# Kernel tuning notes

Measured on AMD Instinct MI355X. Metric: run time of the kernel, lower is better.

## Reference

```python
import jax, jax.numpy as jnp
import numpy as np

B, L, K, E, D, H = 16, 512, 48, 128, 384, 128

def _gelu(x):
    return jax.nn.gelu(x, approximate=False)  # torch nn.GELU default is erf-based

def setup_inputs() -> dict:
    key = jax.random.key(0)
    ks = jax.random.split(key, 16)
    def randn(k, shape, scale=1.0):
        return jax.random.normal(k, shape, dtype=jnp.float32) * scale
    inp = {
        "h_V": randn(ks[0], (B, L, D)),
        "h_E": randn(ks[1], (B, L, K, E)),
        "mask": jnp.ones((B, L), dtype=jnp.float32),
        "fw1": randn(ks[2], (E, D), 1.0 / np.sqrt(E)),
        "fb1": randn(ks[3], (D,), 0.02),
        "fw2": randn(ks[4], (D, D), 1.0 / np.sqrt(D)),
        "fb2": randn(ks[5], (D,), 0.02),
        "hw1": randn(ks[6], (D, H), 1.0 / np.sqrt(D)),
        "hb1": randn(ks[7], (H,), 0.02),
        "hw2": randn(ks[8], (H, H // 2), 1.0 / np.sqrt(H)),
        "hb2": randn(ks[9], (H // 2,), 0.02),
        "hw3": randn(ks[10], (H // 2, 1), 1.0 / np.sqrt(H // 2)),
        "hb3": randn(ks[11], (1,), 0.02),
        "E_idx": jax.random.randint(ks[12], (B, L, K), 0, L),
    }
    return inp

def reference(h_V, h_E, mask, fw1, fb1, fw2, fb2, hw1, hb1, hw2, hb2, hw3, hb3, E_idx):
    # CFConv: edge-conditioned filters [B,L,K,D]
    W = _gelu(_gelu(h_E @ fw1 + fb1) @ fw2 + fb2)
    # gather_nodes: x_j[b,l,k,:] = h_V[b, E_idx[b,l,k], :]
    x_j = jax.vmap(lambda x, idx: x[idx])(h_V, E_idx)  # [B,L,K,D]
    h = jnp.sum(x_j * W, axis=2)  # weighted sum over neighbors -> [B,L,D]
    # mlp_head (dropout = identity at inference)
    h = _gelu(h @ hw1 + hb1)
    h = _gelu(h @ hw2 + hb2)
    dG = (h @ hw3 + hb3)[..., 0]  # [B,L]
    valid_length = jnp.clip(jnp.sum(mask, axis=1), 1.0, None)  # [B]
    return jnp.sum(dG * mask, axis=1) / jnp.sqrt(valid_length)  # [B]
```

## Files before the change

kernel.cpp:

```cpp
#include <hip/hip_runtime.h>
#include <hip/hip_bf16.h>
#include <math.h>

#define NB 16
#define NL 512
#define NK 48
#define NE 128
#define ND 384
#define NH 128

typedef __attribute__((ext_vector_type(8))) short short8;
typedef __attribute__((ext_vector_type(4))) float f32x4;

__device__ __forceinline__ float gelu_fast(float x) {
    float t = x * fmaf(x * x, -0.1029437f, -2.3022087f);
    float e = __builtin_amdgcn_exp2f(t);
    return x * __builtin_amdgcn_rcpf(1.0f + e);
}

__device__ __forceinline__ unsigned short f2bf(float x) {
    union { float f; unsigned u; } v; v.f = x;
    unsigned r = v.u + 0x7fffu + ((v.u >> 16) & 1u);
    return (unsigned short)(r >> 16);
}

__device__ __forceinline__ unsigned short f2bf_rhu(float x) {
    union { float f; unsigned u; } v; v.f = x;
    return (unsigned short)((v.u + 0x8000u) >> 16);
}

__device__ __forceinline__ unsigned pk_bf16(float a, float b) {
    union { float f; unsigned u; } ua, ub; ua.f = a; ub.f = b;
    return __builtin_amdgcn_perm(ua.u + 0x8000u, ub.u + 0x8000u, 0x07060302u);
}

__global__ void pack_weights(const float* __restrict__ fw1,
                             const float* __restrict__ fw2,
                             const float* __restrict__ hw1,
                             const float* __restrict__ hw2,
                             unsigned short* __restrict__ fw1p,
                             unsigned short* __restrict__ fw2p,
                             unsigned short* __restrict__ hw1p,
                             unsigned short* __restrict__ hw2p,
                             float* __restrict__ dGsum) {
    int tid = blockIdx.x * 256 + threadIdx.x;
    if (tid < NB) dGsum[tid] = 0.0f;
    if (tid < NE * ND) {
        int k = tid / ND, n = tid % ND;
        int dst = (((k >> 5) * 24 + (n >> 4)) * 64 + ((k >> 3) & 3) * 16 + (n & 15)) * 8 + (k & 7);
        fw1p[dst] = f2bf(fw1[tid]);
    } else if (tid < NE * ND + ND * ND) {
        int i = tid - NE * ND;
        int k = i / ND, n = i % ND;
        int dst = (((k >> 5) * 24 + (n >> 4)) * 64 + ((k >> 3) & 3) * 16 + (n & 15)) * 8 + (k & 7);
        fw2p[dst] = f2bf(fw2[i]);
    } else if (tid < NE * ND + ND * ND + ND * NH) {
        int i = tid - (NE * ND + ND * ND);
        int k = i / NH, n = i % NH;
        int dst = (((k >> 5) * 8 + (n >> 4)) * 64 + ((k >> 3) & 3) * 16 + (n & 15)) * 8 + (k & 7);
        hw1p[dst] = f2bf(hw1[i]);
    } else if (tid < NE * ND + ND * ND + ND * NH + NH * (NH / 2)) {
        int i = tid - (NE * ND + ND * ND + ND * NH);
        int k = i / (NH / 2), n = i % (NH / 2);
        int dst = (((k >> 5) * 4 + (n >> 4)) * 64 + ((k >> 3) & 3) * 16 + (n & 15)) * 8 + (k & 7);
        hw2p[dst] = f2bf(hw2[i]);
    }
}

__global__ __launch_bounds__(256, 2) void cfconv_kernel(
    const float* __restrict__ h_V, const float* __restrict__ h_E,
    const float* __restrict__ fb1, const float* __restrict__ fb2,
    const unsigned short* __restrict__ fw1p,
    const unsigned short* __restrict__ fw2p,
    const int* __restrict__ E_idx, unsigned short* __restrict__ hbufB)
{
    __shared__ unsigned short smem[96 * 392];
    __shared__ int rowoff_s[96];

    const int t = threadIdx.x;
    const int wave = t >> 6, lane = t & 63;
    const int quad = lane >> 4, l16 = lane & 15;
    const int bl0 = blockIdx.x * 2;
    const int wn0 = wave * 96;

    if (t < 96) {
        int g = t / 48, k = t - g * 48;
        int bl = bl0 + g;
        int idx = E_idx[bl * NK + k];
        rowoff_s[t] = ((bl >> 9) * NL + idx) * ND;
    }

    {
        const float4* src = (const float4*)(h_E + (size_t)bl0 * (NK * NE));
        #pragma unroll
        for (int i = 0; i < 12; i++) {
            int v = i * 256 + t;
            float4 d = src[v];
            int r = v >> 5;
            int c = (v & 31) * 4;
            uint2 u;
            u.x = pk_bf16(d.y, d.x);
            u.y = pk_bf16(d.w, d.z);
            *(uint2*)&smem[r * 136 + c] = u;
        }
    }
    __syncthreads();

    f32x4 acc[6][6];

    #pragma unroll
    for (int mt = 0; mt < 6; mt++)
        #pragma unroll
        for (int nt = 0; nt < 6; nt++)
            acc[mt][nt] = (f32x4){0.f, 0.f, 0.f, 0.f};

    #pragma unroll
    for (int kt = 0; kt < 4; kt++) {
        short8 bfrag[6], afrag[6];
        #pragma unroll
        for (int nt = 0; nt < 6; nt++)
            bfrag[nt] = *(const short8*)(fw1p + (size_t)((kt * 24 + (wn0 >> 4) + nt) * 64 + lane) * 8);
        #pragma unroll
        for (int mt = 0; mt < 6; mt++)
            afrag[mt] = *(const short8*)&smem[(mt * 16 + l16) * 136 + kt * 32 + quad * 8];
        #pragma unroll
        for (int mt = 0; mt < 6; mt++)
            #pragma unroll
            for (int nt = 0; nt < 6; nt++)
                acc[mt][nt] = __builtin_amdgcn_mfma_f32_16x16x32_bf16(
                    afrag[mt], bfrag[nt], acc[mt][nt], 0, 0, 0);
    }
    __syncthreads();

    #pragma unroll
    for (int nt = 0; nt < 6; nt++) {
        int col = wn0 + nt * 16 + l16;
        float b1 = fb1[col];
        #pragma unroll
        for (int mt = 0; mt < 6; mt++) {
            int rowb = mt * 16 + quad * 4;
            #pragma unroll
            for (int r = 0; r < 4; r++)
                smem[(rowb + r) * 392 + col] = f2bf_rhu(gelu_fast(acc[mt][nt][r] + b1));
        }
    }
    __syncthreads();

    #pragma unroll
    for (int mt = 0; mt < 6; mt++)
        #pragma unroll
        for (int nt = 0; nt < 6; nt++)
            acc[mt][nt] = (f32x4){0.f, 0.f, 0.f, 0.f};

    for (int kt = 0; kt < 12; kt++) {
        short8 bfrag[6], afrag[6];
        #pragma unroll
        for (int nt = 0; nt < 6; nt++)
            bfrag[nt] = *(const short8*)(fw2p + (size_t)((kt * 24 + (wn0 >> 4) + nt) * 64 + lane) * 8);
        #pragma unroll
        for (int mt = 0; mt < 6; mt++)
            afrag[mt] = *(const short8*)&smem[(mt * 16 + l16) * 392 + kt * 32 + quad * 8];
        #pragma unroll
        for (int mt = 0; mt < 6; mt++)
            #pragma unroll
            for (int nt = 0; nt < 6; nt++)
                acc[mt][nt] = __builtin_amdgcn_mfma_f32_16x16x32_bf16(
                    afrag[mt], bfrag[nt], acc[mt][nt], 0, 0, 0);
    }

    float b2v[6];
    #pragma unroll
    for (int nt = 0; nt < 6; nt++) b2v[nt] = fb2[wn0 + nt * 16 + l16];

    #pragma unroll
    for (int g = 0; g < 2; g++) {
        const float* pv[12];
        #pragma unroll
        for (int mm = 0; mm < 3; mm++)
            #pragma unroll
            for (int r = 0; r < 4; r++)
                pv[mm * 4 + r] = h_V + rowoff_s[(g * 3 + mm) * 16 + quad * 4 + r] + wn0 + l16;

        #pragma unroll
        for (int nt = 0; nt < 6; nt++) {
            float s = 0.f;
            #pragma unroll
            for (int mm = 0; mm < 3; mm++) {
                #pragma unroll
                for (int r = 0; r < 4; r++) {
                    float w = gelu_fast(acc[g * 3 + mm][nt][r] + b2v[nt]);
                    s = fmaf(w, pv[mm * 4 + r][nt * 16], s);
                }
            }
            s += __shfl_xor(s, 16, 64);
            s += __shfl_xor(s, 32, 64);
            if (lane < 16)
                hbufB[(size_t)(bl0 + g) * ND + wn0 + nt * 16 + lane] = f2bf(s);
        }
    }
}

__global__ __launch_bounds__(64) void head_kernel(
    const unsigned short* __restrict__ hbufB,
    const unsigned short* __restrict__ hw1p, const float* __restrict__ hb1,
    const unsigned short* __restrict__ hw2p, const float* __restrict__ hb2,
    const float* __restrict__ hw3, const float* __restrict__ hb3,
    const float* __restrict__ mask, float* __restrict__ dGsum)
{
    __shared__ unsigned short T1[16 * 136];
    const int lane = threadIdx.x;
    const int quad = lane >> 4, l16 = lane & 15;
    const int row0 = blockIdx.x * 16;

    f32x4 acc1[8];
    #pragma unroll
    for (int nt = 0; nt < 8; nt++) acc1[nt] = (f32x4){0.f, 0.f, 0.f, 0.f};

    for (int kt = 0; kt < 12; kt++) {
        short8 a = *(const short8*)(hbufB + (size_t)(row0 + l16) * ND + kt * 32 + quad * 8);
        #pragma unroll
        for (int nt = 0; nt < 8; nt++) {
            short8 b = *(const short8*)(hw1p + (size_t)((kt * 8 + nt) * 64 + lane) * 8);
            acc1[nt] = __builtin_amdgcn_mfma_f32_16x16x32_bf16(a, b, acc1[nt], 0, 0, 0);
        }
    }

    #pragma unroll
    for (int nt = 0; nt < 8; nt++) {
        int col = nt * 16 + l16;
        float b1 = hb1[col];
        #pragma unroll
        for (int r = 0; r < 4; r++)
            T1[(quad * 4 + r) * 136 + col] = f2bf_rhu(gelu_fast(acc1[nt][r] + b1));
    }
    __syncthreads();

    f32x4 acc2[4];
    #pragma unroll
    for (int nt = 0; nt < 4; nt++) acc2[nt] = (f32x4){0.f, 0.f, 0.f, 0.f};

    #pragma unroll
    for (int kt = 0; kt < 4; kt++) {
        short8 a = *(const short8*)&T1[l16 * 136 + kt * 32 + quad * 8];
        #pragma unroll
        for (int nt = 0; nt < 4; nt++) {
            short8 b = *(const short8*)(hw2p + (size_t)((kt * 4 + nt) * 64 + lane) * 8);
            acc2[nt] = __builtin_amdgcn_mfma_f32_16x16x32_bf16(a, b, acc2[nt], 0, 0, 0);
        }
    }

    float w3[4], b2[4];
    #pragma unroll
    for (int nt = 0; nt < 4; nt++) { w3[nt] = hw3[nt * 16 + l16]; b2[nt] = hb2[nt * 16 + l16]; }

    float dsum = 0.f;
    const float hb3v = hb3[0];
    #pragma unroll
    for (int r = 0; r < 4; r++) {
        float pr = 0.f;
        #pragma unroll
        for (int nt = 0; nt < 4; nt++)
            pr = fmaf(gelu_fast(acc2[nt][r] + b2[nt]), w3[nt], pr);
        pr += __shfl_xor(pr, 1, 64);
        pr += __shfl_xor(pr, 2, 64);
        pr += __shfl_xor(pr, 4, 64);
        pr += __shfl_xor(pr, 8, 64);
        if (l16 == 0) {
            int grow = row0 + quad * 4 + r;
            dsum = fmaf(pr + hb3v, mask[grow], dsum);
        }
    }
    dsum += __shfl_xor(dsum, 16, 64);
    dsum += __shfl_xor(dsum, 32, 64);
    if (lane == 0) atomicAdd(&dGsum[row0 >> 9], dsum);
}

__global__ void finalize_kernel(const float* __restrict__ dGsum,
                                const float* __restrict__ mask,
                                float* __restrict__ out) {
    int t = threadIdx.x;
    int b = t >> 4, j = t & 15;
    float ms = 0.f;
    for (int l = j; l < NL; l += 16) ms += mask[b * NL + l];
    ms += __shfl_xor(ms, 1, 64);
    ms += __shfl_xor(ms, 2, 64);
    ms += __shfl_xor(ms, 4, 64);
    ms += __shfl_xor(ms, 8, 64);
    if (j == 0) {
        ms = fmaxf(ms, 1.0f);
        out[b] = dGsum[b] / sqrtf(ms);
    }
}

extern "C" void kernel_launch(void* const* d_in, const int* in_sizes, int n_in,
                              void* d_out, int out_size, void* d_ws, size_t ws_size,
                              hipStream_t stream) {
    const float* h_V  = (const float*)d_in[0];
    const float* h_E  = (const float*)d_in[1];
    const float* mask = (const float*)d_in[2];
    const float* fw1  = (const float*)d_in[3];
    const float* fb1  = (const float*)d_in[4];
    const float* fw2  = (const float*)d_in[5];
    const float* fb2  = (const float*)d_in[6];
    const float* hw1  = (const float*)d_in[7];
    const float* hb1  = (const float*)d_in[8];
    const float* hw2  = (const float*)d_in[9];
    const float* hb2  = (const float*)d_in[10];
    const float* hw3  = (const float*)d_in[11];
    const float* hb3  = (const float*)d_in[12];
    const int*   E_idx = (const int*)d_in[13];
    float* out = (float*)d_out;

    char* ws = (char*)d_ws;
    unsigned short* fw1p = (unsigned short*)ws;
    unsigned short* fw2p = (unsigned short*)(ws + 98304);
    unsigned short* hw1p = (unsigned short*)(ws + 393216);
    unsigned short* hw2p = (unsigned short*)(ws + 491520);
    float* dGsum = (float*)(ws + 507904);
    unsigned short* hbufB = (unsigned short*)(ws + 512000);

    pack_weights<<<992, 256, 0, stream>>>(fw1, fw2, hw1, hw2, fw1p, fw2p, hw1p, hw2p, dGsum);
    cfconv_kernel<<<(NB * NL) / 2, 256, 0, stream>>>(h_V, h_E, fb1, fb2, fw1p, fw2p, E_idx, hbufB);
    head_kernel<<<(NB * NL) / 16, 64, 0, stream>>>(hbufB, hw1p, hb1, hw2p, hb2, hw3, hb3, mask, dGsum);
    finalize_kernel<<<1, 256, 0, stream>>>(dGsum, mask, out);
}
```

Measured before the change: 501.2 us.

## Double-buffer fw2 fragment loads and batch h_V gathers in the epilogue

The second GEMM loop is restructured so the global loads of the next k-step's fw2 B-fragments go into an alternate register buffer while the current step's MFMAs issue, hiding global-load latency behind the matrix work. The epilogue now loads all 24 gathered h_V values per row group into registers up front, then runs the GELU and multiply-accumulate, so the scattered gathers overlap instead of being serialized with the arithmetic. Both changes raise register pressure, which may reduce occupancy or cause spills in a kernel that already holds a 6x6 accumulator tile.

Result: faster. 465.4 us (-7.2%).

```diff
diff --git a/kernel.cpp b/kernel.cpp
--- a/kernel.cpp
+++ b/kernel.cpp
@@ -152,50 +152,79 @@
         for (int nt = 0; nt < 6; nt++)
             acc[mt][nt] = (f32x4){0.f, 0.f, 0.f, 0.f};
 
-    for (int kt = 0; kt < 12; kt++) {
-        short8 bfrag[6], afrag[6];
-        #pragma unroll
-        for (int nt = 0; nt < 6; nt++)
-            bfrag[nt] = *(const short8*)(fw2p + (size_t)((kt * 24 + (wn0 >> 4) + nt) * 64 + lane) * 8);
-        #pragma unroll
-        for (int mt = 0; mt < 6; mt++)
-            afrag[mt] = *(const short8*)&smem[(mt * 16 + l16) * 392 + kt * 32 + quad * 8];
-        #pragma unroll
-        for (int mt = 0; mt < 6; mt++)
+    {
+        short8 b0[6], b1[6], af[6];
+        #define LOADB(kt, bf)                                                            \
+            _Pragma("unroll")                                                            \
+            for (int nt = 0; nt < 6; nt++)                                               \
+                bf[nt] = *(const short8*)(fw2p +                                         \
+                    (size_t)(((kt) * 24 + (wn0 >> 4) + nt) * 64 + lane) * 8);
+        #define LOADA(kt)                                                                \
+            _Pragma("unroll")                                                            \
+            for (int mt = 0; mt < 6; mt++)                                               \
+                af[mt] = *(const short8*)&smem[(mt * 16 + l16) * 392 + (kt) * 32 + quad * 8];
+        #define MFMAS(bf)                                                                \
+            _Pragma("unroll")                                                            \
+            for (int mt = 0; mt < 6; mt++)                                               \
+                _Pragma("unroll")                                                        \
+                for (int nt = 0; nt < 6; nt++)                                           \
+                    acc[mt][nt] = __builtin_amdgcn_mfma_f32_16x16x32_bf16(               \
+                        af[mt], bf[nt], acc[mt][nt], 0, 0, 0);
+
+        LOADB(0, b0);
+        for (int kt = 0; kt < 10; kt += 2) {
+            LOADB(kt + 1, b1);
+            LOADA(kt);
+            MFMAS(b0);
+            LOADB(kt + 2, b0);
+            LOADA(kt + 1);
+            MFMAS(b1);
+        }
+        LOADB(11, b1);
+        LOADA(10);
+        MFMAS(b0);
+        LOADA(11);
+        MFMAS(b1);
+        #undef LOADB
+        #undef LOADA
+        #undef MFMAS
+    }
+
+    float b2v[6];
+    #pragma unroll
+    for (int nt = 0; nt < 6; nt++) b2v[nt] = fb2[wn0 + nt * 16 + l16];
+
+    #pragma unroll
+    for (int g = 0; g < 2; g++) {
+        float s[6] = {0.f, 0.f, 0.f, 0.f, 0.f, 0.f};
+        #pragma unroll
+        for (int mm = 0; mm < 3; mm++) {
+            const int rb = (g * 3 + mm) * 16 + quad * 4;
+            const float* p0 = h_V + rowoff_s[rb + 0] + wn0 + l16;
+            const float* p1 = h_V + rowoff_s[rb + 1] + wn0 + l16;
+            const float* p2 = h_V + rowoff_s[rb + 2] + wn0 + l16;
+            const float* p3 = h_V + rowoff_s[rb + 3] + wn0 + l16;
+            float xv[6][4];
+            #pragma unroll
+            for (int nt = 0; nt < 6; nt++) {
+                xv[nt][0] = p0[nt * 16];
+                xv[nt][1] = p1[nt * 16];
+                xv[nt][2] = p2[nt * 16];
+                xv[nt][3] = p3[nt * 16];
+            }
             #pragma unroll
             for (int nt = 0; nt < 6; nt++)
-                acc[mt][nt] = __builtin_amdgcn_mfma_f32_16x16x32_bf16(
-                    afrag[mt], bfrag[nt], acc[mt][nt], 0, 0, 0);
-    }
-
-    float b2v[6];
-    #pragma unroll
-    for (int nt = 0; nt < 6; nt++) b2v[nt] = fb2[wn0 + nt * 16 + l16];
-
-    #pragma unroll
-    for (int g = 0; g < 2; g++) {
-        const float* pv[12];
-        #pragma unroll
-        for (int mm = 0; mm < 3; mm++)
-            #pragma unroll
-            for (int r = 0; r < 4; r++)
-                pv[mm * 4 + r] = h_V + rowoff_s[(g * 3 + mm) * 16 + quad * 4 + r] + wn0 + l16;
-
+                #pragma unroll
+                for (int r = 0; r < 4; r++)
+                    s[nt] = fmaf(gelu_fast(acc[g * 3 + mm][nt][r] + b2v[nt]), xv[nt][r], s[nt]);
+        }
         #pragma unroll
         for (int nt = 0; nt < 6; nt++) {
-            float s = 0.f;
-            #pragma unroll
-            for (int mm = 0; mm < 3; mm++) {
-                #pragma unroll
-                for (int r = 0; r < 4; r++) {
-                    float w = gelu_fast(acc[g * 3 + mm][nt][r] + b2v[nt]);
-                    s = fmaf(w, pv[mm * 4 + r][nt * 16], s);
-                }
-            }
-            s += __shfl_xor(s, 16, 64);
-            s += __shfl_xor(s, 32, 64);
+            float v = s[nt];
+            v += __shfl_xor(v, 16, 64);
+            v += __shfl_xor(v, 32, 64);
             if (lane < 16)
-                hbufB[(size_t)(bl0 + g) * ND + wn0 + nt * 16 + lane] = f2bf(s);
+                hbufB[(size_t)(bl0 + g) * ND + wn0 + nt * 16 + lane] = f2bf(v);
         }
     }
 }
```
